# Kernel tuning notes

Hardware: AMD Instinct MI355X
Metric: run time of the kernel (lower is better)

The kernel has to match this reference:

```python
import jax, jax.numpy as jnp
import numpy as np

NUM_HEADS = 8
SIZE_Q = 512
SIZE_K = 512
SIZE_V = 512
B, S = 2, 2048


def setup_inputs() -> dict:
    key = jax.random.key(0)
    ks = jax.random.split(key, 16)
    Hk = SIZE_K  # num_heads * head_size_k
    Hv = SIZE_V  # num_heads * head_size_v
    inp = {
        "k": jax.random.normal(ks[0], (B, S, SIZE_K), jnp.float32),
        "v": jax.random.normal(ks[1], (B, S, SIZE_V), jnp.float32),
        "q": jax.random.normal(ks[2], (B, S, SIZE_Q), jnp.float32),
        "mask": jax.random.randint(ks[3], (S, S), 0, 2).astype(jnp.bool_),
        "spatial_bias": jax.random.normal(ks[4], (1, NUM_HEADS, S, S), jnp.float32),
        # Linear params stored as [in, out]; y = x @ W + b
        "Wq": jax.random.normal(ks[5], (SIZE_Q, Hk), jnp.float32) / np.sqrt(SIZE_Q),
        "bq": jnp.zeros((Hk,), jnp.float32),
        "Wk": jax.random.normal(ks[6], (SIZE_K, Hk), jnp.float32) / np.sqrt(SIZE_K),
        "bk": jnp.zeros((Hk,), jnp.float32),
        "Wv": jax.random.normal(ks[7], (SIZE_V, Hv), jnp.float32) / np.sqrt(SIZE_V),
        "bv": jnp.zeros((Hv,), jnp.float32),
        "Wo": jax.random.normal(ks[8], (Hv, SIZE_V), jnp.float32) / np.sqrt(Hv),
        "bo": jnp.zeros((SIZE_V,), jnp.float32),
    }
    return inp


def reference(k, v, q, mask, spatial_bias, Wq, bq, Wk, bk, Wv, bv, Wo, bo):
    batch, sk = k.shape[0], k.shape[1]
    sq = q.shape[1]
    hdk = Wk.shape[1] // NUM_HEADS
    hdv = Wv.shape[1] // NUM_HEADS
    # QKV projections -> [B, H, S, hd]
    kp = (k @ Wk + bk).reshape(batch, sk, NUM_HEADS, hdk).transpose(0, 2, 1, 3)
    vp = (v @ Wv + bv).reshape(batch, sk, NUM_HEADS, hdv).transpose(0, 2, 1, 3)
    qp = (q @ Wq + bq).reshape(batch, sq, NUM_HEADS, hdk).transpose(0, 2, 1, 3)
    qp = qp / jnp.sqrt(jnp.asarray(hdk, qp.dtype))
    # Scores with additive spatial bias and boolean mask (2D mask -> [1,1,S,S])
    scores = jnp.einsum("bhqd,bhkd->bhqk", qp, kp) + spatial_bias
    scores = jnp.where(mask[None, None, :, :], scores, -jnp.inf)
    attn = jax.nn.softmax(scores, axis=-1)  # dropout=0 (eval)
    ctx = jnp.einsum("bhqk,bhkd->bhqd", attn, vp)
    ctx = ctx.transpose(0, 2, 1, 3).reshape(batch, sq, NUM_HEADS * hdv)
    return ctx @ Wo + bo
```

## Files before the change

### kernel.cpp

```cpp
#include <hip/hip_runtime.h>
#include <hip/hip_bf16.h>

#define S_LEN 2048
#define NH 8
#define HD 64
#define CH 512
#define NEG_BIG (-3.0e38f)
#define KHALF 1024
#define CTXP_STRIDE (2 * NH * S_LEN * HD)
#define ML_STRIDE   (2 * NH * S_LEN)
#define OUTP_STRIDE (4096 * 512)

typedef __bf16 bf16;
typedef bf16 bf16x8 __attribute__((ext_vector_type(8)));
typedef bf16 bf16x4 __attribute__((ext_vector_type(4)));
typedef float floatx4 __attribute__((ext_vector_type(4)));

typedef const unsigned int __attribute__((address_space(1)))* gas1_t;
typedef unsigned int __attribute__((address_space(3)))* las3_t;
__device__ __forceinline__ void gll16(const void* g, void* l) {
    __builtin_amdgcn_global_load_lds((gas1_t)g, (las3_t)l, 16, 0, 0);
}

__global__ void detect_mask_kernel(const unsigned char* __restrict__ mb,
                                   int* __restrict__ flag_out) {
    __shared__ int s1, s3;
    if (threadIdx.x == 0) { s1 = 0; s3 = 0; }
    __syncthreads();
    int any1 = 0, any3 = 0;
    int base = threadIdx.x * 16;
    for (int i = base; i < base + 16; ++i) {
        unsigned char bch = mb[i];
        int m = i & 3;
        if (bch != 0) {
            if (m == 1) any1 = 1;
            if (m == 2 || m == 3) any3 = 1;
        }
    }
    if (any1) atomicOr(&s1, 1);
    if (any3) atomicOr(&s3, 1);
    __syncthreads();
    if (threadIdx.x == 0) {
        int f = 0;
        if (s1) f = 1;
        else if (s3) f = 2;
        *flag_out = f;
    }
}

__global__ __launch_bounds__(256) void prep_weights_kernel(
    const float* __restrict__ Wq, const float* __restrict__ Wk,
    const float* __restrict__ Wv, const float* __restrict__ Wo,
    bf16* __restrict__ WThi, bf16* __restrict__ WTlo)
{
    __shared__ float tile[64][65];
    const int t = threadIdx.x;
    const int n0 = blockIdx.x * 64;
    const int k0 = blockIdx.y * 64;
    const int mat = blockIdx.z;
    const float* W = (mat == 0) ? Wq : (mat == 1) ? Wk : (mat == 2) ? Wv : Wo;
    bf16* hi = WThi + (size_t)mat * (CH * CH);
    bf16* lo = WTlo + (size_t)mat * (CH * CH);
#pragma unroll
    for (int i = 0; i < 4; ++i) {
        int row = (t >> 4) + 16 * i;
        int c4 = (t & 15) << 2;
        float4 f = *(const float4*)(W + (size_t)(k0 + row) * CH + n0 + c4);
        tile[row][c4 + 0] = f.x; tile[row][c4 + 1] = f.y;
        tile[row][c4 + 2] = f.z; tile[row][c4 + 3] = f.w;
    }
    __syncthreads();
#pragma unroll
    for (int i = 0; i < 4; ++i) {
        int nr = (t >> 4) + 16 * i;
        int k4 = (t & 15) << 2;
        bf16x4 h, l;
#pragma unroll
        for (int j = 0; j < 4; ++j) {
            float x = tile[k4 + j][nr];
            bf16 hv = (bf16)x;
            h[j] = hv;
            l[j] = (bf16)(x - (float)hv);
        }
        *(bf16x4*)(hi + (size_t)(n0 + nr) * CH + k0 + k4) = h;
        *(bf16x4*)(lo + (size_t)(n0 + nr) * CH + k0 + k4) = l;
    }
}

__device__ __forceinline__ void gemm_bf16_tile(
    bf16* __restrict__ As_hi, bf16* __restrict__ As_lo,
    bf16* __restrict__ Bs_hi, bf16* __restrict__ Bs_lo,
    const float* __restrict__ IN, const bf16* __restrict__ WThi,
    const bf16* __restrict__ WTlo, const float* __restrict__ BI,
    float* __restrict__ OUT, bf16* __restrict__ OBF,
    const float* __restrict__ ML, float scale, int mode,
    int kbeg, int kiters)
{
    const int t = threadIdx.x;
    const int w = t >> 6;
    const int lane = t & 63;
    const int m16 = lane & 15;
    const int quad = lane >> 4;
    const int m0 = blockIdx.y * 64;
    const int n0 = blockIdx.x * 128;

    const int arow = t >> 2;
    const int ac8  = (t & 3) << 3;
    const int brow = t >> 1;
    const int bkc  = (t & 1) << 4;

    floatx4 acc[8];
#pragma unroll
    for (int ni = 0; ni < 8; ++ni) {
        acc[ni][0] = 0.f; acc[ni][1] = 0.f;
        acc[ni][2] = 0.f; acc[ni][3] = 0.f;
    }

    float4 af[2];
    bf16x8 pbh[2], pbl[2];

    auto loadA = [&](int k0) {
        if (ML) {
            int col = k0 + ac8;
            int hh = col >> 6, dd = col & 63;
            int row = m0 + arow;
            int bb = row >> 11, ss = row & (S_LEN - 1);
            size_t prow = ((size_t)bb * NH + hh) * S_LEN + ss;
            float m0v = ML[prow * 2],                 l0v = ML[prow * 2 + 1];
            float m1v = ML[(ML_STRIDE + prow) * 2],   l1v = ML[(ML_STRIDE + prow) * 2 + 1];
            float mx = fmaxf(m0v, m1v);
            float e0 = __expf(m0v - mx), e1 = __expf(m1v - mx);
            float den = e0 * l0v + e1 * l1v;
            float inv = den > 0.f ? 1.f / den : 0.f;
            float a0 = e0 * inv, a1 = e1 * inv;
            const float* p0 = IN + prow * HD + dd;
            const float* p1 = p0 + CTXP_STRIDE;
#pragma unroll
            for (int j = 0; j < 2; ++j) {
                float4 c0 = ((const float4*)p0)[j];
                float4 c1 = ((const float4*)p1)[j];
                af[j].x = a0 * c0.x + a1 * c1.x;
                af[j].y = a0 * c0.y + a1 * c1.y;
                af[j].z = a0 * c0.z + a1 * c1.z;
                af[j].w = a0 * c0.w + a1 * c1.w;
            }
        } else {
            const float* p = IN + (size_t)(m0 + arow) * CH + k0 + ac8;
            af[0] = ((const float4*)p)[0];
            af[1] = ((const float4*)p)[1];
        }
    };
    auto loadB = [&](int k0) {
        const bf16* ph = WThi + (size_t)(n0 + brow) * CH + k0 + bkc;
        const bf16* pl = WTlo + (size_t)(n0 + brow) * CH + k0 + bkc;
        pbh[0] = ((const bf16x8*)ph)[0]; pbh[1] = ((const bf16x8*)ph)[1];
        pbl[0] = ((const bf16x8*)pl)[0]; pbl[1] = ((const bf16x8*)pl)[1];
    };
    auto stage = [&]() {
        bf16x8 h, l;
#pragma unroll
        for (int j = 0; j < 8; ++j) {
            float x = ((const float*)&af[0])[j];
            bf16 hv = (bf16)x;
            h[j] = hv;
            l[j] = (bf16)(x - (float)hv);
        }
        *(bf16x8*)&As_hi[arow * 40 + ac8] = h;
        *(bf16x8*)&As_lo[arow * 40 + ac8] = l;
        *(bf16x8*)&Bs_hi[brow * 40 + bkc + 0] = pbh[0];
        *(bf16x8*)&Bs_hi[brow * 40 + bkc + 8] = pbh[1];
        *(bf16x8*)&Bs_lo[brow * 40 + bkc + 0] = pbl[0];
        *(bf16x8*)&Bs_lo[brow * 40 + bkc + 8] = pbl[1];
    };

    loadA(kbeg); loadB(kbeg);
    for (int ks = 0; ks < kiters; ++ks) {
        __syncthreads();
        stage();
        __syncthreads();
        if (ks + 1 < kiters) { loadA(kbeg + 32 * (ks + 1)); loadB(kbeg + 32 * (ks + 1)); }

        bf16x8 bh[8], bl[8];
#pragma unroll
        for (int ni = 0; ni < 8; ++ni) {
            bh[ni] = *(const bf16x8*)&Bs_hi[(16 * ni + m16) * 40 + 8 * quad];
            bl[ni] = *(const bf16x8*)&Bs_lo[(16 * ni + m16) * 40 + 8 * quad];
        }
        bf16x8 ah = *(const bf16x8*)&As_hi[(16 * w + m16) * 40 + 8 * quad];
        bf16x8 al = *(const bf16x8*)&As_lo[(16 * w + m16) * 40 + 8 * quad];
#pragma unroll
        for (int ni = 0; ni < 8; ++ni) {
            acc[ni] = __builtin_amdgcn_mfma_f32_16x16x32_bf16(ah, bh[ni], acc[ni], 0, 0, 0);
            acc[ni] = __builtin_amdgcn_mfma_f32_16x16x32_bf16(ah, bl[ni], acc[ni], 0, 0, 0);
            acc[ni] = __builtin_amdgcn_mfma_f32_16x16x32_bf16(al, bh[ni], acc[ni], 0, 0, 0);
        }
    }

#pragma unroll
    for (int r = 0; r < 4; ++r) {
        int row = m0 + 16 * w + 4 * quad + r;
        int bb = row >> 11;
        int ss = row & (S_LEN - 1);
#pragma unroll
        for (int ni = 0; ni < 8; ++ni) {
            int col = n0 + 16 * ni + m16;
            float v = BI ? (acc[ni][r] + BI[col]) * scale
                         : acc[ni][r] * scale;
            if (mode == 0) {
                int hh = col >> 6, dd = col & 63;
                OUT[(((size_t)bb * NH + hh) * S_LEN + ss) * HD + dd] = v;
            } else if (mode == 3) {
                int hh = col >> 6, dd = col & 63;
                OBF[((size_t)(bb * NH + hh) * S_LEN + ss) * HD
                    + (((dd >> 3) ^ (ss & 7)) << 3) + (dd & 7)] = (bf16)v;
            } else if (mode == 4) {
                int hh = col >> 6, dd = col & 63;
                OBF[((size_t)(bb * NH + hh) * HD + dd) * S_LEN
                    + (ss & ~63) + ((((ss >> 3) & 7) ^ (dd & 7)) << 3) + (ss & 7)] = (bf16)v;
            } else {
                OUT[(size_t)row * CH + col] = v;
            }
        }
    }
}

__global__ __launch_bounds__(256, 4) void qkv_gemm_kernel(
    const float* __restrict__ q_in, const float* __restrict__ k_in,
    const float* __restrict__ v_in,
    const bf16* __restrict__ WThi, const bf16* __restrict__ WTlo,
    const float* __restrict__ bq, const float* __restrict__ bk,
    const float* __restrict__ bv,
    float* __restrict__ qp, bf16* __restrict__ kswz, bf16* __restrict__ vswz)
{
    __shared__ __attribute__((aligned(16))) bf16 As_hi[64 * 40];
    __shared__ __attribute__((aligned(16))) bf16 As_lo[64 * 40];
    __shared__ __attribute__((aligned(16))) bf16 Bs_hi[128 * 40];
    __shared__ __attribute__((aligned(16))) bf16 Bs_lo[128 * 40];
    int z = blockIdx.z;
    if (z == 0)
        gemm_bf16_tile(As_hi, As_lo, Bs_hi, Bs_lo, q_in,
                       WThi, WTlo, bq, qp, nullptr, nullptr, 0.125f, 0, 0, 16);
    else if (z == 1)
        gemm_bf16_tile(As_hi, As_lo, Bs_hi, Bs_lo, k_in,
                       WThi + (size_t)CH * CH, WTlo + (size_t)CH * CH, bk,
                       nullptr, kswz, nullptr, 1.0f, 3, 0, 16);
    else
        gemm_bf16_tile(As_hi, As_lo, Bs_hi, Bs_lo, v_in,
                       WThi + (size_t)2 * CH * CH, WTlo + (size_t)2 * CH * CH, bv,
                       nullptr, vswz, nullptr, 1.0f, 4, 0, 16);
}

__global__ __launch_bounds__(256, 4) void out_gemm_kernel(
    const float* __restrict__ ctxp, const float* __restrict__ ml,
    const bf16* __restrict__ WThi, const bf16* __restrict__ WTlo,
    float* __restrict__ outp)
{
    __shared__ __attribute__((aligned(16))) bf16 As_hi[64 * 40];
    __shared__ __attribute__((aligned(16))) bf16 As_lo[64 * 40];
    __shared__ __attribute__((aligned(16))) bf16 Bs_hi[128 * 40];
    __shared__ __attribute__((aligned(16))) bf16 Bs_lo[128 * 40];
    int z = blockIdx.z;
    gemm_bf16_tile(As_hi, As_lo, Bs_hi, Bs_lo, ctxp,
                   WThi + (size_t)3 * CH * CH, WTlo + (size_t)3 * CH * CH,
                   nullptr, outp + (size_t)z * OUTP_STRIDE, nullptr, ml,
                   1.0f, 2, z * 256, 8);
}

__global__ __launch_bounds__(256) void add_out_kernel(
    const float* __restrict__ outp, const float* __restrict__ bo,
    float* __restrict__ out)
{
    int idx = blockIdx.x * 256 + threadIdx.x;
    int col4 = (idx & 127) << 2;
    float4 a = ((const float4*)outp)[idx];
    float4 b = ((const float4*)(outp + OUTP_STRIDE))[idx];
    float4 c = *(const float4*)(bo + col4);
    float4 o;
    o.x = a.x + b.x + c.x;
    o.y = a.y + b.y + c.y;
    o.z = a.z + b.z + c.z;
    o.w = a.w + b.w + c.w;
    ((float4*)out)[idx] = o;
}

__global__ __launch_bounds__(256, 4) void attn_kernel(
    const float* __restrict__ qp, const bf16* __restrict__ kswz,
    const bf16* __restrict__ vswz, const float* __restrict__ bias,
    const void* __restrict__ mask, const int* __restrict__ flagp,
    float* __restrict__ ctxp, float* __restrict__ ml)
{
    __shared__ __attribute__((aligned(16))) bf16 Kt[2][64 * 64];
    __shared__ __attribute__((aligned(16))) bf16 Vt[2][64 * 64];
    __shared__ __attribute__((aligned(16))) bf16 Pbf[64 * 72];

    const int t    = threadIdx.x;
    const int w    = t >> 6;
    const int lane = t & 63;
    const int m16  = lane & 15;
    const int quad = lane >> 4;
    const int mx7  = m16 & 7;

    const int p  = blockIdx.x + 32 * (blockIdx.y + 8 * blockIdx.z);
    const int l  = (p & 7) * 128 + (p >> 3);
    const int b  = l & 1;
    const int kz = (l >> 1) & 1;
    const int h  = (l >> 2) & 7;
    const int qi = l >> 5;

    const int q0   = qi * 64;
    const int bh   = b * NH + h;
    const int flag = *flagp;
    const int kbeg = kz * KHALF;

    bf16x8 qf[2];
    {
        const float* qrow =
            qp + ((size_t)bh * S_LEN + q0 + 16 * w + m16) * HD + 8 * quad;
#pragma unroll
        for (int c = 0; c < 2; ++c) {
            float4 f0 = *(const float4*)(qrow + 32 * c);
            float4 f1 = *(const float4*)(qrow + 32 * c + 4);
            bf16x8 v;
            v[0] = (bf16)f0.x; v[1] = (bf16)f0.y; v[2] = (bf16)f0.z; v[3] = (bf16)f0.w;
            v[4] = (bf16)f1.x; v[5] = (bf16)f1.y; v[6] = (bf16)f1.z; v[7] = (bf16)f1.w;
            qf[c] = v;
        }
    }

    floatx4 ctxa[4];
    float mrow[4], lrow[4];
#pragma unroll
    for (int tt = 0; tt < 4; ++tt) { ctxa[tt][0]=0.f; ctxa[tt][1]=0.f; ctxa[tt][2]=0.f; ctxa[tt][3]=0.f; }
#pragma unroll
    for (int r = 0; r < 4; ++r) { mrow[r] = NEG_BIG; lrow[r] = 0.f; }

    const int qrow0 = q0 + 16 * w + 4 * quad;
    const float* bbase = bias + ((size_t)h * S_LEN + qrow0) * S_LEN + m16;
    const unsigned char* mb8  = (const unsigned char*)mask + (size_t)qrow0 * S_LEN + m16;
    const unsigned int*  mb32 = (const unsigned int*)mask  + (size_t)qrow0 * S_LEN + m16;

    float bnext[16]; unsigned mnext[16]; float mb[16];
    auto prefetchBM = [&](int k0) {
        if (flag == 1) {
#pragma unroll
            for (int r = 0; r < 4; ++r)
#pragma unroll
                for (int tt = 0; tt < 4; ++tt)
                    mnext[4 * r + tt] = mb8[(size_t)r * S_LEN + k0 + 16 * tt];
        } else {
#pragma unroll
            for (int r = 0; r < 4; ++r)
#pragma unroll
                for (int tt = 0; tt < 4; ++tt)
                    mnext[4 * r + tt] = mb32[(size_t)r * S_LEN + k0 + 16 * tt];
        }
#pragma unroll
        for (int r = 0; r < 4; ++r)
#pragma unroll
            for (int tt = 0; tt < 4; ++tt)
                bnext[4 * r + tt] = bbase[(size_t)r * S_LEN + k0 + 16 * tt];
    };

    const bf16* kb = kswz + (size_t)bh * S_LEN * HD;
    const bf16* vb = vswz + (size_t)bh * HD * S_LEN;
    const int lrow8 = lane >> 3;
    const int lcol8 = (lane & 7) * 8;

    auto stageKV = [&](int k0, int buf) {
#pragma unroll
        for (int i = 0; i < 2; ++i) {
            int c = 2 * w + i;
            int row = 8 * c + lrow8;
            gll16(kb + (size_t)(k0 + row) * HD + lcol8, &Kt[buf][c * 512]);
            gll16(vb + (size_t)row * S_LEN + k0 + lcol8, &Vt[buf][c * 512]);
        }
    };

    prefetchBM(kbeg);
    stageKV(kbeg, 0);
    __syncthreads();
    int cur = 0;

    for (int k0 = kbeg; k0 < kbeg + KHALF; k0 += 64) {
        const bool more = (k0 + 64 < kbeg + KHALF);
        if (more) stageKV(k0 + 64, cur ^ 1);

#pragma unroll
        for (int j = 0; j < 16; ++j) mb[j] = mnext[j] ? bnext[j] : NEG_BIG;
        if (more) prefetchBM(k0 + 64);

        const bf16* Kc = Kt[cur];
        const bf16* Vc = Vt[cur];
        floatx4 sc[4];
#pragma unroll
        for (int tt = 0; tt < 4; ++tt) { sc[tt][0]=0.f; sc[tt][1]=0.f; sc[tt][2]=0.f; sc[tt][3]=0.f; }
#pragma unroll
        for (int st = 0; st < 2; ++st)
#pragma unroll
            for (int tt = 0; tt < 4; ++tt) {
                bf16x8 kf = *(const bf16x8*)&Kc[(16 * tt + m16) * 64
                                                + (((quad + 4 * st) ^ mx7) << 3)];
                sc[tt] = __builtin_amdgcn_mfma_f32_16x16x32_bf16(qf[st], kf, sc[tt], 0, 0, 0);
            }

        float alpha[4];
#pragma unroll
        for (int r = 0; r < 4; ++r) {
            int lrowq = 16 * w + 4 * quad + r;
            float s[4];
#pragma unroll
            for (int tt = 0; tt < 4; ++tt)
                s[tt] = sc[tt][r] + mb[4 * r + tt];
            float mx = fmaxf(fmaxf(s[0], s[1]), fmaxf(s[2], s[3]));
            mx = fmaxf(mx, __shfl_xor(mx, 1));
            mx = fmaxf(mx, __shfl_xor(mx, 2));
            mx = fmaxf(mx, __shfl_xor(mx, 4));
            mx = fmaxf(mx, __shfl_xor(mx, 8));
            float mnew = fmaxf(mrow[r], mx);
            float al = __expf(mrow[r] - mnew);
            float ls = 0.f;
#pragma unroll
            for (int tt = 0; tt < 4; ++tt) {
                float px = (s[tt] <= -1e37f) ? 0.f : __expf(s[tt] - mnew);
                ls += px;
                Pbf[lrowq * 72 + 16 * tt + m16] = (bf16)px;
            }
            ls += __shfl_xor(ls, 1);
            ls += __shfl_xor(ls, 2);
            ls += __shfl_xor(ls, 4);
            ls += __shfl_xor(ls, 8);
            lrow[r] = lrow[r] * al + ls;
            mrow[r] = mnew;
            alpha[r] = al;
        }
#pragma unroll
        for (int tt = 0; tt < 4; ++tt)
#pragma unroll
            for (int r = 0; r < 4; ++r) ctxa[tt][r] *= alpha[r];

#pragma unroll
        for (int st = 0; st < 2; ++st) {
            bf16x8 pf = *(const bf16x8*)&Pbf[(16 * w + m16) * 72 + 8 * quad + 32 * st];
#pragma unroll
            for (int tt = 0; tt < 4; ++tt) {
                bf16x8 vf = *(const bf16x8*)&Vc[(16 * tt + m16) * 64
                                                + (((quad + 4 * st) ^ mx7) << 3)];
                ctxa[tt] = __builtin_amdgcn_mfma_f32_16x16x32_bf16(pf, vf, ctxa[tt], 0, 0, 0);
            }
        }

        __syncthreads();
        cur ^= 1;
    }

    float* cp = ctxp + (size_t)kz * CTXP_STRIDE;
#pragma unroll
    for (int r = 0; r < 4; ++r) {
        int grow = q0 + 16 * w + 4 * quad + r;
        size_t prow = (size_t)bh * S_LEN + grow;
#pragma unroll
        for (int tt = 0; tt < 4; ++tt)
            cp[prow * HD + 16 * tt + m16] = ctxa[tt][r];
        if (m16 == 0) {
            ml[((size_t)kz * ML_STRIDE + prow) * 2 + 0] = mrow[r];
            ml[((size_t)kz * ML_STRIDE + prow) * 2 + 1] = lrow[r];
        }
    }
}

extern "C" void kernel_launch(void* const* d_in, const int* in_sizes, int n_in,
                              void* d_out, int out_size, void* d_ws, size_t ws_size,
                              hipStream_t stream) {
    const float* k_in = (const float*)d_in[0];
    const float* v_in = (const float*)d_in[1];
    const float* q_in = (const float*)d_in[2];
    const void*  mask = d_in[3];
    const float* bias = (const float*)d_in[4];
    const float* Wq = (const float*)d_in[5];
    const float* bq = (const float*)d_in[6];
    const float* Wk = (const float*)d_in[7];
    const float* bk = (const float*)d_in[8];
    const float* Wv = (const float*)d_in[9];
    const float* bv = (const float*)d_in[10];
    const float* Wo = (const float*)d_in[11];
    const float* bo = (const float*)d_in[12];
    float* out = (float*)d_out;

    char* base = (char*)d_ws;
    float* qp   = (float*)(base);
    float* ctxp = (float*)(base + (8u  << 20));
    float* mlb  = (float*)(base + (24u << 20));
    bf16*  kswz = (bf16*) (base + (25u << 20));
    bf16*  vswz = (bf16*) (base + (29u << 20));
    bf16*  WThi = (bf16*) (base + (33u << 20));
    bf16*  WTlo = (bf16*) (base + (35u << 20));
    float* outp = (float*)(base + (37u << 20));
    int*   flag = (int*)  (base + (53u << 20));

    detect_mask_kernel<<<1, 256, 0, stream>>>((const unsigned char*)mask, flag);
    prep_weights_kernel<<<dim3(8, 8, 4), 256, 0, stream>>>(
        Wq, Wk, Wv, Wo, WThi, WTlo);
    qkv_gemm_kernel<<<dim3(4, 64, 3), 256, 0, stream>>>(
        q_in, k_in, v_in, WThi, WTlo, bq, bk, bv, qp, kswz, vswz);
    attn_kernel<<<dim3(32, 8, 4), 256, 0, stream>>>(
        qp, kswz, vswz, bias, mask, flag, ctxp, mlb);
    out_gemm_kernel<<<dim3(4, 64, 2), 256, 0, stream>>>(
        ctxp, mlb, WThi, WTlo, outp);
    add_out_kernel<<<2048, 256, 0, stream>>>(outp, bo, out);
}
```

Baseline: 357.8 us.

## Process 128 query rows per attention block and hoist merge weights in out GEMM

The attention kernel now handles two 64-row query sub-tiles per block, so each staged K/V tile in shared memory feeds twice as many query rows and the grid is halved. Mask bits are packed into a bitmask to save registers, and the launch-bounds occupancy hint drops from 4 to 3 blocks to allow the larger register footprint. Separately, the out-GEMM precomputes the split-K softmax merge weights for its four heads once, instead of reloading m/l and recomputing exponentials on every A-tile load. The risks are lower occupancy, more register pressure, and fewer blocks to spread across the GPU's compute units.

```diff
diff --git a/kernel.cpp b/kernel.cpp
--- a/kernel.cpp
+++ b/kernel.cpp
@@ -119,21 +119,37 @@
     float4 af[2];
     bf16x8 pbh[2], pbl[2];
 
-    auto loadA = [&](int k0) {
-        if (ML) {
-            int col = k0 + ac8;
-            int hh = col >> 6, dd = col & 63;
-            int row = m0 + arow;
-            int bb = row >> 11, ss = row & (S_LEN - 1);
-            size_t prow = ((size_t)bb * NH + hh) * S_LEN + ss;
-            float m0v = ML[prow * 2],                 l0v = ML[prow * 2 + 1];
-            float m1v = ML[(ML_STRIDE + prow) * 2],   l1v = ML[(ML_STRIDE + prow) * 2 + 1];
+    float a0c0 = 0.f, a1c0 = 0.f, a0c1 = 0.f, a1c1 = 0.f;
+    float a0c2 = 0.f, a1c2 = 0.f, a0c3 = 0.f, a1c3 = 0.f;
+    size_t mlpb = 0;
+    const int hb = kbeg >> 6;
+    if (ML) {
+        int row = m0 + arow;
+        int bb = row >> 11, ss = row & (S_LEN - 1);
+        mlpb = (size_t)bb * NH * S_LEN + ss;
+        auto mlw = [&](int hh, float& a0, float& a1) {
+            size_t prow = mlpb + (size_t)hh * S_LEN;
+            float m0v = ML[prow * 2],               l0v = ML[prow * 2 + 1];
+            float m1v = ML[(ML_STRIDE + prow) * 2], l1v = ML[(ML_STRIDE + prow) * 2 + 1];
             float mx = fmaxf(m0v, m1v);
             float e0 = __expf(m0v - mx), e1 = __expf(m1v - mx);
             float den = e0 * l0v + e1 * l1v;
             float inv = den > 0.f ? 1.f / den : 0.f;
-            float a0 = e0 * inv, a1 = e1 * inv;
-            const float* p0 = IN + prow * HD + dd;
+            a0 = e0 * inv; a1 = e1 * inv;
+        };
+        mlw(hb + 0, a0c0, a1c0);
+        mlw(hb + 1, a0c1, a1c1);
+        mlw(hb + 2, a0c2, a1c2);
+        mlw(hb + 3, a0c3, a1c3);
+    }
+
+    auto loadA = [&](int k0) {
+        if (ML) {
+            int hl = (k0 >> 6) - hb;
+            int dd = (k0 & 63) + ac8;
+            float a0 = hl == 0 ? a0c0 : hl == 1 ? a0c1 : hl == 2 ? a0c2 : a0c3;
+            float a1 = hl == 0 ? a1c0 : hl == 1 ? a1c1 : hl == 2 ? a1c2 : a1c3;
+            const float* p0 = IN + (mlpb + (size_t)(hb + hl) * S_LEN) * HD + dd;
             const float* p1 = p0 + CTXP_STRIDE;
 #pragma unroll
             for (int j = 0; j < 2; ++j) {
@@ -283,7 +299,7 @@
     ((float4*)out)[idx] = o;
 }
 
-__global__ __launch_bounds__(256, 4) void attn_kernel(
+__global__ __launch_bounds__(256, 3) void attn_kernel(
     const float* __restrict__ qp, const bf16* __restrict__ kswz,
     const bf16* __restrict__ vswz, const float* __restrict__ bias,
     const void* __restrict__ mask, const int* __restrict__ flagp,
@@ -300,22 +316,23 @@
     const int quad = lane >> 4;
     const int mx7  = m16 & 7;
 
-    const int p  = blockIdx.x + 32 * (blockIdx.y + 8 * blockIdx.z);
-    const int l  = (p & 7) * 128 + (p >> 3);
+    const int p  = blockIdx.x + 16 * (blockIdx.y + 8 * blockIdx.z);
+    const int l  = (p & 7) * 64 + (p >> 3);
     const int b  = l & 1;
     const int kz = (l >> 1) & 1;
     const int h  = (l >> 2) & 7;
     const int qi = l >> 5;
 
-    const int q0   = qi * 64;
+    const int q0   = qi * 128;
     const int bh   = b * NH + h;
     const int flag = *flagp;
     const int kbeg = kz * KHALF;
 
-    bf16x8 qf[2];
-    {
+    bf16x8 qf[4];
+#pragma unroll
+    for (int sub = 0; sub < 2; ++sub) {
         const float* qrow =
-            qp + ((size_t)bh * S_LEN + q0 + 16 * w + m16) * HD + 8 * quad;
+            qp + ((size_t)bh * S_LEN + q0 + sub * 64 + 16 * w + m16) * HD + 8 * quad;
 #pragma unroll
         for (int c = 0; c < 2; ++c) {
             float4 f0 = *(const float4*)(qrow + 32 * c);
@@ -323,42 +340,53 @@
             bf16x8 v;
             v[0] = (bf16)f0.x; v[1] = (bf16)f0.y; v[2] = (bf16)f0.z; v[3] = (bf16)f0.w;
             v[4] = (bf16)f1.x; v[5] = (bf16)f1.y; v[6] = (bf16)f1.z; v[7] = (bf16)f1.w;
-            qf[c] = v;
-        }
-    }
-
-    floatx4 ctxa[4];
-    float mrow[4], lrow[4];
-#pragma unroll
-    for (int tt = 0; tt < 4; ++tt) { ctxa[tt][0]=0.f; ctxa[tt][1]=0.f; ctxa[tt][2]=0.f; ctxa[tt][3]=0.f; }
-#pragma unroll
-    for (int r = 0; r < 4; ++r) { mrow[r] = NEG_BIG; lrow[r] = 0.f; }
+            qf[sub * 2 + c] = v;
+        }
+    }
+
+    floatx4 ctxa[2][4];
+    float mrow[2][4], lrow[2][4];
+#pragma unroll
+    for (int sub = 0; sub < 2; ++sub)
+#pragma unroll
+        for (int tt = 0; tt < 4; ++tt) {
+            ctxa[sub][tt][0] = 0.f; ctxa[sub][tt][1] = 0.f;
+            ctxa[sub][tt][2] = 0.f; ctxa[sub][tt][3] = 0.f;
+        }
+#pragma unroll
+    for (int sub = 0; sub < 2; ++sub)
+#pragma unroll
+        for (int r = 0; r < 4; ++r) { mrow[sub][r] = NEG_BIG; lrow[sub][r] = 0.f; }
 
     const int qrow0 = q0 + 16 * w + 4 * quad;
     const float* bbase = bias + ((size_t)h * S_LEN + qrow0) * S_LEN + m16;
     const unsigned char* mb8  = (const unsigned char*)mask + (size_t)qrow0 * S_LEN + m16;
     const unsigned int*  mb32 = (const unsigned int*)mask  + (size_t)qrow0 * S_LEN + m16;
 
-    float bnext[16]; unsigned mnext[16]; float mb[16];
-    auto prefetchBM = [&](int k0) {
+    float bnext[32];
+    unsigned bits[2];
+    auto prefetchBM = [&](int k0, int sub) {
+        const size_t ro = (size_t)(sub * 64);
+        unsigned bt = 0;
         if (flag == 1) {
 #pragma unroll
             for (int r = 0; r < 4; ++r)
 #pragma unroll
                 for (int tt = 0; tt < 4; ++tt)
-                    mnext[4 * r + tt] = mb8[(size_t)r * S_LEN + k0 + 16 * tt];
+                    if (mb8[(ro + r) * S_LEN + k0 + 16 * tt]) bt |= 1u << (4 * r + tt);
         } else {
 #pragma unroll
             for (int r = 0; r < 4; ++r)
 #pragma unroll
                 for (int tt = 0; tt < 4; ++tt)
-                    mnext[4 * r + tt] = mb32[(size_t)r * S_LEN + k0 + 16 * tt];
-        }
+                    if (mb32[(ro + r) * S_LEN + k0 + 16 * tt]) bt |= 1u << (4 * r + tt);
+        }
+        bits[sub] = bt;
 #pragma unroll
         for (int r = 0; r < 4; ++r)
 #pragma unroll
             for (int tt = 0; tt < 4; ++tt)
-                bnext[4 * r + tt] = bbase[(size_t)r * S_LEN + k0 + 16 * tt];
+                bnext[sub * 16 + 4 * r + tt] = bbase[(ro + r) * S_LEN + k0 + 16 * tt];
     };
 
     const bf16* kb = kswz + (size_t)bh * S_LEN * HD;
@@ -376,7 +404,8 @@
         }
     };
 
-    prefetchBM(kbeg);
+    prefetchBM(kbeg, 0);
+    prefetchBM(kbeg, 1);
     stageKV(kbeg, 0);
     __syncthreads();
     int cur = 0;
@@ -385,67 +414,76 @@
         const bool more = (k0 + 64 < kbeg + KHALF);
         if (more) stageKV(k0 + 64, cur ^ 1);
 
-#pragma unroll
-        for (int j = 0; j < 16; ++j) mb[j] = mnext[j] ? bnext[j] : NEG_BIG;
-        if (more) prefetchBM(k0 + 64);
-
         const bf16* Kc = Kt[cur];
         const bf16* Vc = Vt[cur];
-        floatx4 sc[4];
-#pragma unroll
-        for (int tt = 0; tt < 4; ++tt) { sc[tt][0]=0.f; sc[tt][1]=0.f; sc[tt][2]=0.f; sc[tt][3]=0.f; }
-#pragma unroll
-        for (int st = 0; st < 2; ++st)
-#pragma unroll
-            for (int tt = 0; tt < 4; ++tt) {
-                bf16x8 kf = *(const bf16x8*)&Kc[(16 * tt + m16) * 64
-                                                + (((quad + 4 * st) ^ mx7) << 3)];
-                sc[tt] = __builtin_amdgcn_mfma_f32_16x16x32_bf16(qf[st], kf, sc[tt], 0, 0, 0);
+
+#pragma unroll
+        for (int sub = 0; sub < 2; ++sub) {
+            floatx4 sc[4];
+#pragma unroll
+            for (int tt = 0; tt < 4; ++tt) { sc[tt][0]=0.f; sc[tt][1]=0.f; sc[tt][2]=0.f; sc[tt][3]=0.f; }
+#pragma unroll
+            for (int st = 0; st < 2; ++st)
+#pragma unroll
+                for (int tt = 0; tt < 4; ++tt) {
+                    bf16x8 kf = *(const bf16x8*)&Kc[(16 * tt + m16) * 64
+                                                    + (((quad + 4 * st) ^ mx7) << 3)];
+                    sc[tt] = __builtin_amdgcn_mfma_f32_16x16x32_bf16(qf[sub * 2 + st], kf, sc[tt], 0, 0, 0);
+                }
+
+            float mbv[16];
+            {
+                unsigned bt = bits[sub];
+#pragma unroll
+                for (int j = 0; j < 16; ++j)
+                    mbv[j] = ((bt >> j) & 1u) ? bnext[sub * 16 + j] : NEG_BIG;
             }
-
-        float alpha[4];
-#pragma unroll
-        for (int r = 0; r < 4; ++r) {
-            int lrowq = 16 * w + 4 * quad + r;
-            float s[4];
+            if (more) prefetchBM(k0 + 64, sub);
+
+            float alpha[4];
+#pragma unroll
+            for (int r = 0; r < 4; ++r) {
+                int lrowq = 16 * w + 4 * quad + r;
+                float s[4];
+#pragma unroll
+                for (int tt = 0; tt < 4; ++tt)
+                    s[tt] = sc[tt][r] + mbv[4 * r + tt];
+                float mx = fmaxf(fmaxf(s[0], s[1]), fmaxf(s[2], s[3]));
+                mx = fmaxf(mx, __shfl_xor(mx, 1));
+                mx = fmaxf(mx, __shfl_xor(mx, 2));
+                mx = fmaxf(mx, __shfl_xor(mx, 4));
+                mx = fmaxf(mx, __shfl_xor(mx, 8));
+                float mnew = fmaxf(mrow[sub][r], mx);
+                float al = __expf(mrow[sub][r] - mnew);
+                float ls = 0.f;
+#pragma unroll
+                for (int tt = 0; tt < 4; ++tt) {
+                    float px = (s[tt] <= -1e37f) ? 0.f : __expf(s[tt] - mnew);
+                    ls += px;
+                    Pbf[lrowq * 72 + 16 * tt + m16] = (bf16)px;
+                }
+                ls += __shfl_xor(ls, 1);
+                ls += __shfl_xor(ls, 2);
+                ls += __shfl_xor(ls, 4);
+                ls += __shfl_xor(ls, 8);
+                lrow[sub][r] = lrow[sub][r] * al + ls;
+                mrow[sub][r] = mnew;
+                alpha[r] = al;
+            }
 #pragma unroll
             for (int tt = 0; tt < 4; ++tt)
-                s[tt] = sc[tt][r] + mb[4 * r + tt];
-            float mx = fmaxf(fmaxf(s[0], s[1]), fmaxf(s[2], s[3]));
-            mx = fmaxf(mx, __shfl_xor(mx, 1));
-            mx = fmaxf(mx, __shfl_xor(mx, 2));
-            mx = fmaxf(mx, __shfl_xor(mx, 4));
-            mx = fmaxf(mx, __shfl_xor(mx, 8));
-            float mnew = fmaxf(mrow[r], mx);
-            float al = __expf(mrow[r] - mnew);
-            float ls = 0.f;
-#pragma unroll
-            for (int tt = 0; tt < 4; ++tt) {
-                float px = (s[tt] <= -1e37f) ? 0.f : __expf(s[tt] - mnew);
-                ls += px;
-                Pbf[lrowq * 72 + 16 * tt + m16] = (bf16)px;
-            }
-            ls += __shfl_xor(ls, 1);
-            ls += __shfl_xor(ls, 2);
-            ls += __shfl_xor(ls, 4);
-            ls += __shfl_xor(ls, 8);
-            lrow[r] = lrow[r] * al + ls;
-            mrow[r] = mnew;
-            alpha[r] = al;
-        }
-#pragma unroll
-        for (int tt = 0; tt < 4; ++tt)
-#pragma unroll
-            for (int r = 0; r < 4; ++r) ctxa[tt][r] *= alpha[r];
-
-#pragma unroll
-        for (int st = 0; st < 2; ++st) {
-            bf16x8 pf = *(const bf16x8*)&Pbf[(16 * w + m16) * 72 + 8 * quad + 32 * st];
-#pragma unroll
-            for (int tt = 0; tt < 4; ++tt) {
-                bf16x8 vf = *(const bf16x8*)&Vc[(16 * tt + m16) * 64
-                                                + (((quad + 4 * st) ^ mx7) << 3)];
-                ctxa[tt] = __builtin_amdgcn_mfma_f32_16x16x32_bf16(pf, vf, ctxa[tt], 0, 0, 0);
+#pragma unroll
+                for (int r = 0; r < 4; ++r) ctxa[sub][tt][r] *= alpha[r];
+
+#pragma unroll
+            for (int st = 0; st < 2; ++st) {
+                bf16x8 pf = *(const bf16x8*)&Pbf[(16 * w + m16) * 72 + 8 * quad + 32 * st];
+#pragma unroll
+                for (int tt = 0; tt < 4; ++tt) {
+                    bf16x8 vf = *(const bf16x8*)&Vc[(16 * tt + m16) * 64
+                                                    + (((quad + 4 * st) ^ mx7) << 3)];
+                    ctxa[sub][tt] = __builtin_amdgcn_mfma_f32_16x16x32_bf16(pf, vf, ctxa[sub][tt], 0, 0, 0);
+                }
             }
         }
 
@@ -455,15 +493,17 @@
 
     float* cp = ctxp + (size_t)kz * CTXP_STRIDE;
 #pragma unroll
+    for (int sub = 0; sub < 2; ++sub)
+#pragma unroll
     for (int r = 0; r < 4; ++r) {
-        int grow = q0 + 16 * w + 4 * quad + r;
+        int grow = q0 + sub * 64 + 16 * w + 4 * quad + r;
         size_t prow = (size_t)bh * S_LEN + grow;
 #pragma unroll
         for (int tt = 0; tt < 4; ++tt)
-            cp[prow * HD + 16 * tt + m16] = ctxa[tt][r];
+            cp[prow * HD + 16 * tt + m16] = ctxa[sub][tt][r];
         if (m16 == 0) {
-            ml[((size_t)kz * ML_STRIDE + prow) * 2 + 0] = mrow[r];
-            ml[((size_t)kz * ML_STRIDE + prow) * 2 + 1] = lrow[r];
+            ml[((size_t)kz * ML_STRIDE + prow) * 2 + 0] = mrow[sub][r];
+            ml[((size_t)kz * ML_STRIDE + prow) * 2 + 1] = lrow[sub][r];
         }
     }
 }
@@ -502,7 +542,7 @@
         Wq, Wk, Wv, Wo, WThi, WTlo);
     qkv_gemm_kernel<<<dim3(4, 64, 3), 256, 0, stream>>>(
         q_in, k_in, v_in, WThi, WTlo, bq, bk, bv, qp, kswz, vswz);
-    attn_kernel<<<dim3(32, 8, 4), 256, 0, stream>>>(
+    attn_kernel<<<dim3(16, 8, 4), 256, 0, stream>>>(
         qp, kswz, vswz, bias, mask, flag, ctxp, mlb);
     out_gemm_kernel<<<dim3(4, 64, 2), 256, 0, stream>>>(
         ctxp, mlb, WThi, WTlo, outp);
```

After: 588.2 us. +64.4%, slower.
